# Optimization experiments

Hardware: AMD Instinct MI355X
Metric: run time of the kernel (lower is better)

Reference implementation:

```python
import jax, jax.numpy as jnp
import numpy as np

B, H, W, C = 4, 64, 64, 96
EXPAND = 2
D_INNER = EXPAND * C  # 192
N = 16   # d_state
K = 4    # scan directions
DT_RANK = int(np.ceil(C / 16))  # 6


def setup_inputs() -> dict:
    key = jax.random.key(0)
    ks = jax.random.split(key, 8)
    def rn(k, shape, scale=0.02):
        return jax.random.normal(k, shape, dtype=jnp.float32) * scale
    return {
        "x": jax.random.normal(ks[0], (B, H, W, C), dtype=jnp.float32),
        "ln_g": jnp.ones((C,), jnp.float32),
        "ln_b": jnp.zeros((C,), jnp.float32),
        "in_proj_w": rn(ks[1], (C, 2 * D_INNER)),
        "in_proj_b": jnp.zeros((2 * D_INNER,), jnp.float32),
        "conv_w": rn(ks[2], (D_INNER, 1, 3, 3), 0.1),
        "conv_b": jnp.zeros((D_INNER,), jnp.float32),
        "x_proj_w": rn(ks[3], (K, DT_RANK + 2 * N, D_INNER)),
        "dt_proj_w": rn(ks[4], (K, D_INNER, DT_RANK), 0.1),
        "dt_proj_b": rn(ks[5], (K, D_INNER), 0.1),
        "A_logs": jnp.log(jnp.tile(jnp.arange(1, N + 1, dtype=jnp.float32)[None, :], (K * D_INNER, 1))),
        "Ds": jnp.ones((K * D_INNER,), jnp.float32),
        "out_norm_g": jnp.ones((D_INNER,), jnp.float32),
        "out_norm_b": jnp.zeros((D_INNER,), jnp.float32),
        "out_proj_w": rn(ks[6], (D_INNER, C)),
        "out_proj_b": jnp.zeros((C,), jnp.float32),
    }


def _ln(x, g, b, eps):
    mu = x.mean(-1, keepdims=True)
    var = jnp.mean((x - mu) ** 2, axis=-1, keepdims=True)
    return (x - mu) * jax.lax.rsqrt(var + eps) * g + b


def _vss_forward(x, ln_g, ln_b, in_proj_w, in_proj_b, conv_w, conv_b,
                 x_proj_w, dt_proj_w, dt_proj_b, A_logs, Ds,
                 out_norm_g, out_norm_b, out_proj_w, out_proj_b):
    Bb, Hh, Ww, Cc = x.shape
    L = Hh * Ww
    d = D_INNER
    # ln_1 (eps=1e-6), then SS2D on channels-first layout
    xn = _ln(x, ln_g, ln_b, 1e-6)
    xz = jnp.einsum('bhwc,ce->bhwe', xn, in_proj_w) + in_proj_b
    xi, z = jnp.split(xz, 2, axis=-1)
    xi = xi.transpose(0, 3, 1, 2)  # (B, d, H, W)
    xi = jax.lax.conv_general_dilated(
        xi, conv_w, (1, 1), 'SAME', feature_group_count=d,
        dimension_numbers=('NCHW', 'OIHW', 'NCHW'))
    xi = jax.nn.silu(xi + conv_b[None, :, None, None])
    # 4 scan directions: row-major, col-major, and their reverses
    x_hw = xi.reshape(Bb, d, L)
    x_wh = xi.transpose(0, 1, 3, 2).reshape(Bb, d, L)
    xs = jnp.stack([x_hw, x_wh], axis=1)                      # (B,2,d,L)
    xs = jnp.concatenate([xs, jnp.flip(xs, axis=-1)], axis=1)  # (B,K,d,L)
    x_dbl = jnp.einsum('bkdl,kcd->bkcl', xs, x_proj_w)         # (B,K,R+2N,L)
    dt_r = x_dbl[:, :, :DT_RANK]
    Bs = x_dbl[:, :, DT_RANK:DT_RANK + N]                      # (B,K,N,L)
    Cs = x_dbl[:, :, DT_RANK + N:]                             # (B,K,N,L)
    dts = jnp.einsum('bkrl,kdr->bkdl', dt_r, dt_proj_w)
    dts = jax.nn.softplus(dts + dt_proj_b[None, :, :, None])
    A = -jnp.exp(A_logs).reshape(K, d, N)
    Dsk = Ds.reshape(K, d)

    def step(h, inp):
        u_t, dt_t, B_t, C_t = inp                  # (B,K,d),(B,K,d),(B,K,N),(B,K,N)
        dA = jnp.exp(dt_t[..., None] * A)          # (B,K,d,N)
        h = dA * h + (dt_t * u_t)[..., None] * B_t[:, :, None, :]
        y = jnp.einsum('bkdn,bkn->bkd', h, C_t)
        return h, y

    seq = (xs.transpose(3, 0, 1, 2), dts.transpose(3, 0, 1, 2),
           Bs.transpose(3, 0, 1, 2), Cs.transpose(3, 0, 1, 2))
    h0 = jnp.zeros((Bb, K, d, N), xs.dtype)
    _, ys = jax.lax.scan(step, h0, seq)            # ys: (L,B,K,d)
    ys = ys.transpose(1, 2, 3, 0)                  # (B,K,d,L)
    ys = ys + Dsk[None, :, :, None] * xs
    # merge the 4 directions back into one row-major map
    inv_y = jnp.flip(ys[:, 2:4], axis=-1)
    wh_y = ys[:, 1].reshape(Bb, d, Ww, Hh).transpose(0, 1, 3, 2).reshape(Bb, d, L)
    invwh_y = inv_y[:, 1].reshape(Bb, d, Ww, Hh).transpose(0, 1, 3, 2).reshape(Bb, d, L)
    y = ys[:, 0] + inv_y[:, 0] + wh_y + invwh_y    # (B,d,L)
    y = y.transpose(0, 2, 1).reshape(Bb, Hh, Ww, d)
    y = _ln(y, out_norm_g, out_norm_b, 1e-5)
    y = y * jax.nn.silu(z)
    out = jnp.einsum('bhwd,dc->bhwc', y, out_proj_w) + out_proj_b
    return x + out  # residual (drop_path = 0 -> identity)


def reference(x, ln_g, ln_b, in_proj_w, in_proj_b, conv_w, conv_b, x_proj_w,
              dt_proj_w, dt_proj_b, A_logs, Ds, out_norm_g, out_norm_b,
              out_proj_w, out_proj_b):
    return _vss_forward(x, ln_g, ln_b, in_proj_w, in_proj_b, conv_w, conv_b,
                        x_proj_w, dt_proj_w, dt_proj_b, A_logs, Ds,
                        out_norm_g, out_norm_b, out_proj_w, out_proj_b)
```

## Files before the change

### kernel.cpp

```cpp
#include <hip/hip_runtime.h>
#include <math.h>

#define CC   96
#define DIN  192
#define NST  16
#define KDIR 4
#define DTR  6
#define LL   4096
#define BB   4
#define NSEG 128
#define SEGLEN 32
#define XROW 40

#define SZ_BLD ((long)BB*LL*DIN)

__device__ __forceinline__ float sigmoidf_(float x){
    return __builtin_amdgcn_rcpf(1.0f + __expf(-x));
}
__device__ __forceinline__ int whmap(int l){ return ((l & 63) << 6) | (l >> 6); }

__device__ __forceinline__ void dt_and_E(float s, float& dt, float& E){
    const float LOG2E = 1.4426950408889634f;
    const float LN2   = 0.6931471805599453f;
    float sn  = s * LOG2E;
    float t   = __builtin_amdgcn_exp2f(-fabsf(sn));
    float opt = 1.0f + t;
    float r   = __builtin_amdgcn_rcpf(opt);
    E  = (s > 0.f) ? t*r : r;
    dt = LN2 * (fmaxf(sn, 0.f) + __builtin_amdgcn_logf(opt));
}
__device__ __forceinline__ void pow_tree(float E, float* En){
    En[0]=E;
    float E2=E*E;        En[1]=E2;
    En[2]=E2*E;  float E4=E2*E2; En[3]=E4;
    En[4]=E4*E;  En[5]=E4*E2;  En[6]=E4*En[2];
    float E8=E4*E4;      En[7]=E8;
    En[8]=E8*E;  En[9]=E8*E2;  En[10]=E8*En[2]; En[11]=E8*E4;
    En[12]=E8*En[4]; En[13]=E8*En[5]; En[14]=E8*En[6]; En[15]=E8*E8;
}
__device__ __forceinline__ void dir_base(int k, int lg0, int& p0, int& stride){
    switch(k & 3){
        case 0:  p0 = lg0;               stride = 1;   break;
        case 1:  p0 = whmap(lg0);        stride = 64;  break;
        case 2:  p0 = LL - 1 - lg0;      stride = -1;  break;
        default: p0 = whmap(LL-1-lg0);   stride = -64; break;
    }
}

__global__ __launch_bounds__(192) void kA(const float* __restrict__ x,
        const float* __restrict__ lng, const float* __restrict__ lnb,
        const float* __restrict__ W,   const float* __restrict__ bias,
        float* __restrict__ xi, float* __restrict__ z)
{
    __shared__ float xn[16*96];
    __shared__ float sc1[192], sc2[192];
    __shared__ float mu[16], rs[16];
    int t = threadIdx.x;
    long row0 = (long)blockIdx.x * 16;

    for(int q=t; q<16*96; q+=192) xn[q] = x[row0*96 + q];
    __syncthreads();
    {
        int r = t/12, i = t%12;
        float4 v0 = *(const float4*)(&xn[r*96 + i*8]);
        float4 v1 = *(const float4*)(&xn[r*96 + i*8 + 4]);
        float s  = v0.x+v0.y+v0.z+v0.w + v1.x+v1.y+v1.z+v1.w;
        float ss = v0.x*v0.x+v0.y*v0.y+v0.z*v0.z+v0.w*v0.w
                 + v1.x*v1.x+v1.y*v1.y+v1.z*v1.z+v1.w*v1.w;
        sc1[t]=s; sc2[t]=ss;
        __syncthreads();
        if(t<16){
            float S=0.f, SS=0.f;
            for(int j=0;j<12;j++){ S+=sc1[t*12+j]; SS+=sc2[t*12+j]; }
            float m = S*(1.0f/96.0f);
            float var = SS*(1.0f/96.0f) - m*m;
            mu[t]=m; rs[t]=rsqrtf(var + 1e-6f);
        }
        __syncthreads();
    }
    for(int q=t; q<16*96; q+=192){
        int r=q/96, c=q%96;
        xn[q] = (xn[q]-mu[r])*rs[r]*lng[c] + lnb[c];
    }
    __syncthreads();

    float acc0[16], acc1[16];
    #pragma unroll
    for(int r=0;r<16;r++){ acc0[r]=0.f; acc1[r]=0.f; }
    for(int c0=0; c0<96; c0+=4){
        float4 xv[16];
        #pragma unroll
        for(int r=0;r<16;r++) xv[r] = *(const float4*)(&xn[r*96 + c0]);
        #pragma unroll
        for(int j=0;j<4;j++){
            float w0 = W[(c0+j)*384 + t];
            float w1 = W[(c0+j)*384 + t + 192];
            #pragma unroll
            for(int r=0;r<16;r++){
                float xvj = (j==0)?xv[r].x:(j==1)?xv[r].y:(j==2)?xv[r].z:xv[r].w;
                acc0[r] = fmaf(xvj, w0, acc0[r]);
                acc1[r] = fmaf(xvj, w1, acc1[r]);
            }
        }
    }
    float b0 = bias[t], b1 = bias[t+192];
    #pragma unroll
    for(int r=0;r<16;r++){
        xi[(row0+r)*DIN + t] = acc0[r] + b0;
        z [(row0+r)*DIN + t] = acc1[r] + b1;
    }
}

__global__ __launch_bounds__(256) void kB(const float* __restrict__ xi,
        const float* __restrict__ cw, const float* __restrict__ cb,
        float* __restrict__ xc)
{
    long idx = (long)blockIdx.x*256 + threadIdx.x;
    if(idx >= SZ_BLD) return;
    int d = (int)(idx % DIN);
    long rg = idx / DIN;
    int p = (int)(rg % LL); int b = (int)(rg / LL);
    int h = p >> 6, w = p & 63;
    float acc = 0.f;
    #pragma unroll
    for(int dh=0; dh<3; dh++){
        int hh = h + dh - 1;
        if(hh < 0 || hh >= 64) continue;
        #pragma unroll
        for(int dw=0; dw<3; dw++){
            int ww2 = w + dw - 1;
            if(ww2 < 0 || ww2 >= 64) continue;
            acc = fmaf(xi[((long)b*LL + hh*64 + ww2)*DIN + d], cw[d*9 + dh*3 + dw], acc);
        }
    }
    acc += cb[d];
    xc[idx] = acc * sigmoidf_(acc);
}

__global__ __launch_bounds__(320) void kC(const float* __restrict__ xc,
        const float* __restrict__ xw, float* __restrict__ xdbl)
{
    __shared__ float ls[16*192];
    int t = threadIdx.x;
    long row0 = (long)blockIdx.x * 16;
    int b  = (int)(row0 / LL);
    int p0 = (int)(row0 % LL);
    for(int q=t; q<16*192; q+=320) ls[q] = xc[row0*DIN + q];
    __syncthreads();
    if(t < 304){
        int q4 = t / 76;
        int j  = t % 76;
        int k  = j / 38;
        int c  = j % 38;
        const float* wr0 = xw + (long)( k      *38 + c)*192;
        const float* wr1 = xw + (long)((k + 2) *38 + c)*192;
        float acc0[4], acc1[4];
        #pragma unroll
        for(int r=0;r<4;r++){ acc0[r]=0.f; acc1[r]=0.f; }
        int rbase = q4*4;
        for(int d=0; d<192; d+=4){
            float4 w0 = *(const float4*)(wr0 + d);
            float4 w1 = *(const float4*)(wr1 + d);
            #pragma unroll
            for(int r=0;r<4;r++){
                float4 lv = *(const float4*)(&ls[(rbase+r)*192 + d]);
                acc0[r] = fmaf(lv.x,w0.x, fmaf(lv.y,w0.y, fmaf(lv.z,w0.z, fmaf(lv.w,w0.w, acc0[r]))));
                acc1[r] = fmaf(lv.x,w1.x, fmaf(lv.y,w1.y, fmaf(lv.z,w1.z, fmaf(lv.w,w1.w, acc1[r]))));
            }
        }
        int cs = (c < 6) ? c : c + 2;
        long base0 = (long)(b*KDIR + k)*LL;
        long base2 = (long)(b*KDIR + k + 2)*LL;
        #pragma unroll
        for(int r=0;r<4;r++){
            int p  = p0 + rbase + r;
            int lk = (k==0) ? p : whmap(p);
            xdbl[(base0 + lk)*XROW + cs]            = acc0[r];
            xdbl[(base2 + (LL-1-lk))*XROW + cs]     = acc1[r];
        }
    }
}

__global__ __launch_bounds__(192) void kD2(const float* __restrict__ xc,
        const float* __restrict__ xdbl, const float* __restrict__ alog,
        const float* __restrict__ dtw,  const float* __restrict__ dtb,
        float* __restrict__ hend, float* __restrict__ dtsum)
{
    __shared__ float rows[SEGLEN*XROW];
    int t = threadIdx.x;
    int blk = blockIdx.x;
    int bk = blk / NSEG, seg = blk % NSEG;
    int b = bk / KDIR, k = bk % KDIR;
    {
        const float* src = xdbl + ((long)bk*LL + seg*SEGLEN)*XROW;
        for(int q=t; q<SEGLEN*XROW; q+=192) rows[q] = src[q];
    }
    int d = t, kd = k*192 + d;
    float a[16]; bool fast = true;
    #pragma unroll
    for(int n=0;n<16;n++){
        a[n] = -__expf(alog[kd*16 + n]);
        fast = fast && (fabsf(a[n] + (float)(n+1)) < 1e-3f);
    }
    float w6[6];
    #pragma unroll
    for(int r=0;r<6;r++) w6[r] = dtw[kd*6 + r];
    float bdt = dtb[kd];

    int lg0 = seg * SEGLEN;
    int p0, stride; dir_base(k, lg0, p0, stride);
    long addr  = ((long)b*LL + p0)*DIN + d;
    long astep = (long)stride*DIN;

    float h[16];
    #pragma unroll
    for(int n=0;n<16;n++) h[n]=0.f;
    float sdt = 0.f;
    __syncthreads();

    float u = xc[addr];
    for(int i=0; i<SEGLEN; i++){
        const float* row = &rows[i*XROW];
        float s = bdt;
        #pragma unroll
        for(int r=0;r<6;r++) s = fmaf(row[r], w6[r], s);
        float dt, E; dt_and_E(s, dt, E);
        sdt += dt;
        float wi = dt * u;
        float unext = 0.f;
        long addrN = addr + astep;
        if(i+1 < SEGLEN) unext = xc[addrN];
        float En[16];
        if(fast){ pow_tree(E, En); }
        else {
            #pragma unroll
            for(int n=0;n<16;n++) En[n] = __expf(dt * a[n]);
        }
        float Bv[16];
        #pragma unroll
        for(int n=0;n<16;n+=4) *(float4*)(Bv+n) = *(const float4*)(row + 8 + n);
        #pragma unroll
        for(int n=0;n<16;n++) h[n] = fmaf(En[n], h[n], wi*Bv[n]);
        addr = addrN; u = unext;
    }
    long hb = (((long)bk*NSEG + seg)*192 + d)*16;
    #pragma unroll
    for(int n=0;n<16;n+=4)
        *(float4*)(&hend[hb+n]) = make_float4(h[n],h[n+1],h[n+2],h[n+3]);
    dtsum[((long)bk*NSEG + seg)*192 + d] = sdt;
}

__global__ __launch_bounds__(256) void kE3(const float* __restrict__ alog,
        const float* __restrict__ dtsum, float* __restrict__ hx)
{
    int tid = blockIdx.x*256 + threadIdx.x;
    int c     = tid & 15;
    int chain = tid >> 4;
    int n  = chain & 15;
    int d  = (chain >> 4) % 192;
    int bk = chain / 3072;
    int k  = bk & 3;
    float an = -__expf(alog[(k*192 + d)*16 + n]);
    long sbase = (long)bk*NSEG*192  + d;
    long hbase = (long)bk*NSEG*3072 + d*16 + n;
    int seg0 = c*8;

    float P[8], he[8];
    #pragma unroll
    for(int i=0;i<8;i++){
        float sd = dtsum[sbase + (long)(seg0+i)*192];
        he[i]    = hx[hbase + (long)(seg0+i)*3072];
        P[i]     = __expf(an * sd);
    }
    float Pc = 1.f, Hc = 0.f;
    #pragma unroll
    for(int i=0;i<8;i++){
        Hc = fmaf(P[i], Hc, he[i]);
        Pc *= P[i];
    }
    #pragma unroll
    for(int dist=1; dist<16; dist<<=1){
        float Pp = __shfl_up(Pc, dist, 16);
        float Hp = __shfl_up(Hc, dist, 16);
        if(c >= dist){
            Hc = fmaf(Pc, Hp, Hc);
            Pc *= Pp;
        }
    }
    float H = __shfl_up(Hc, 1, 16);
    if(c == 0) H = 0.f;
    #pragma unroll
    for(int i=0;i<8;i++){
        hx[hbase + (long)(seg0+i)*3072] = H;
        H = fmaf(P[i], H, he[i]);
    }
}

__global__ __launch_bounds__(192) void kF2(const float* __restrict__ xc,
        const float* __restrict__ xdbl, const float* __restrict__ alog,
        const float* __restrict__ dtw,  const float* __restrict__ dtb,
        const float* __restrict__ Ds,   const float* __restrict__ Hprev,
        float* __restrict__ ys0, float* __restrict__ ys123)
{
    __shared__ float rows[SEGLEN*XROW];
    int t = threadIdx.x;
    int blk = blockIdx.x;
    int bk = blk / NSEG, seg = blk % NSEG;
    int b = bk / KDIR, k = bk % KDIR;
    {
        const float* src = xdbl + ((long)bk*LL + seg*SEGLEN)*XROW;
        for(int q=t; q<SEGLEN*XROW; q+=192) rows[q] = src[q];
    }
    int d = t, kd = k*192 + d;
    float a[16]; bool fast = true;
    #pragma unroll
    for(int n=0;n<16;n++){
        a[n] = -__expf(alog[kd*16 + n]);
        fast = fast && (fabsf(a[n] + (float)(n+1)) < 1e-3f);
    }
    float w6[6];
    #pragma unroll
    for(int r=0;r<6;r++) w6[r] = dtw[kd*6 + r];
    float bdt = dtb[kd];
    float Dd  = Ds[kd];
    float h[16];
    long hb = (((long)bk*NSEG + seg)*192 + d)*16;
    #pragma unroll
    for(int n=0;n<16;n+=4){
        float4 v = *(const float4*)(&Hprev[hb+n]);
        h[n]=v.x; h[n+1]=v.y; h[n+2]=v.z; h[n+3]=v.w;
    }
    float* ybuf = (k==0) ? ys0 : (ys123 + (long)(k-1)*SZ_BLD);

    int lg0 = seg * SEGLEN;
    int p0, stride; dir_base(k, lg0, p0, stride);
    long addr  = ((long)b*LL + p0)*DIN + d;
    long astep = (long)stride*DIN;
    __syncthreads();

    float u = xc[addr];
    for(int i=0; i<SEGLEN; i++){
        const float* row = &rows[i*XROW];
        float s = bdt;
        #pragma unroll
        for(int r=0;r<6;r++) s = fmaf(row[r], w6[r], s);
        float dt, E; dt_and_E(s, dt, E);
        float wi = dt * u;
        float unext = 0.f;
        long addrN = addr + astep;
        if(i+1 < SEGLEN) unext = xc[addrN];
        float En[16];
        if(fast){ pow_tree(E, En); }
        else {
            #pragma unroll
            for(int n=0;n<16;n++) En[n] = __expf(dt * a[n]);
        }
        float Bv[16], Cv[16];
        #pragma unroll
        for(int n=0;n<16;n+=4){
            *(float4*)(Bv+n) = *(const float4*)(row + 8 + n);
            *(float4*)(Cv+n) = *(const float4*)(row + 24 + n);
        }
        float y = Dd * u;
        #pragma unroll
        for(int n=0;n<16;n++){
            h[n] = fmaf(En[n], h[n], wi*Bv[n]);
            y = fmaf(h[n], Cv[n], y);
        }
        ybuf[addr] = y;
        addr = addrN; u = unext;
    }
}

__global__ __launch_bounds__(384) void kG(const float* __restrict__ ys0,
        const float* __restrict__ ys123, const float* __restrict__ z,
        const float* __restrict__ ong, const float* __restrict__ onb,
        const float* __restrict__ Wout, const float* __restrict__ ob,
        const float* __restrict__ x, float* __restrict__ out)
{
    __shared__ float yb[16*192];
    __shared__ float sc1[384], sc2[384];
    __shared__ float mu[16], rs[16];
    int t = threadIdx.x;
    long row0 = (long)blockIdx.x * 16;

    for(int q=t; q<3072; q+=384){
        long off = row0*DIN + q;
        yb[q] = ys0[off] + ys123[off] + ys123[SZ_BLD + off] + ys123[2*SZ_BLD + off];
    }
    __syncthreads();
    {
        int r = t/24, i = t%24;
        float s=0.f, ss=0.f;
        #pragma unroll
        for(int j=0;j<8;j++){ float v = yb[r*192 + i*8 + j]; s+=v; ss+=v*v; }
        sc1[t]=s; sc2[t]=ss;
        __syncthreads();
        if(t<16){
            float S=0.f, SS=0.f;
            for(int j=0;j<24;j++){ S+=sc1[t*24+j]; SS+=sc2[t*24+j]; }
            float m = S*(1.0f/192.0f);
            float var = SS*(1.0f/192.0f) - m*m;
            mu[t]=m; rs[t]=rsqrtf(var + 1e-5f);
        }
        __syncthreads();
    }
    for(int q=t; q<3072; q+=384){
        int r=q/192, dd=q%192;
        float v = (yb[q]-mu[r])*rs[r]*ong[dd] + onb[dd];
        float zz = z[row0*DIN + q];
        yb[q] = v * (zz * sigmoidf_(zz));
    }
    __syncthreads();
    int c = t % 96, rg4 = t / 96;
    float acc[4] = {0.f,0.f,0.f,0.f};
    for(int dd=0; dd<192; dd++){
        float wv = Wout[dd*96 + c];
        #pragma unroll
        for(int j=0;j<4;j++) acc[j] = fmaf(yb[(rg4*4+j)*192 + dd], wv, acc[j]);
    }
    float bv = ob[c];
    for(int j=0;j<4;j++){
        long row = row0 + rg4*4 + j;
        out[row*96 + c] = x[row*96 + c] + acc[j] + bv;
    }
}

extern "C" void kernel_launch(void* const* d_in, const int* in_sizes, int n_in,
                              void* d_out, int out_size, void* d_ws, size_t ws_size,
                              hipStream_t stream)
{
    const float* x    = (const float*)d_in[0];
    const float* lng  = (const float*)d_in[1];
    const float* lnb  = (const float*)d_in[2];
    const float* ipw  = (const float*)d_in[3];
    const float* ipb  = (const float*)d_in[4];
    const float* cw   = (const float*)d_in[5];
    const float* cb   = (const float*)d_in[6];
    const float* xpw  = (const float*)d_in[7];
    const float* dtw  = (const float*)d_in[8];
    const float* dtb  = (const float*)d_in[9];
    const float* alog = (const float*)d_in[10];
    const float* Ds   = (const float*)d_in[11];
    const float* ong  = (const float*)d_in[12];
    const float* onb  = (const float*)d_in[13];
    const float* opw  = (const float*)d_in[14];
    const float* opb  = (const float*)d_in[15];

    float* ws    = (float*)d_ws;
    float* xi    = ws + 0;
    float* z     = ws + 3145728;
    float* xc    = ws + 6291456;
    float* xdbl  = ws + 9437184;
    float* ys123 = ws + 12058624;
    float* hx    = ws + 21495808;
    float* dtsum = ws + 27787264;
    float* ys0   = xi;
    float* out   = (float*)d_out;

    hipLaunchKernelGGL(kA,  dim3(1024),  dim3(192), 0, stream, x, lng, lnb, ipw, ipb, xi, z);
    hipLaunchKernelGGL(kB,  dim3(12288), dim3(256), 0, stream, xi, cw, cb, xc);
    hipLaunchKernelGGL(kC,  dim3(1024),  dim3(320), 0, stream, xc, xpw, xdbl);
    hipLaunchKernelGGL(kD2, dim3(2048),  dim3(192), 0, stream, xc, xdbl, alog, dtw, dtb,
                       hx, dtsum);
    hipLaunchKernelGGL(kE3, dim3(3072),  dim3(256), 0, stream, alog, dtsum, hx);
    hipLaunchKernelGGL(kF2, dim3(2048),  dim3(192), 0, stream, xc, xdbl, alog, dtw, dtb,
                       Ds, hx, ys0, ys123);
    hipLaunchKernelGGL(kG,  dim3(1024),  dim3(384), 0, stream, ys0, ys123, z, ong, onb,
                       opw, opb, x, out);
}
```

Measured before the change: 328.4 us.

## Transpose x_proj weights and retile kC for coalesced weight loads

Adds a small kernel that transposes the x_proj weight into a [k][d][c] layout, so adjacent threads in kC read adjacent weight elements. kC is retiled to 8 rows per block with 152 active threads, each computing one (direction, channel) output over 8 rows instead of two directions over 4 rows. The aim is coalesced weight reads and higher occupancy, at the cost of an extra launch each call and of dropping the float4 weight loads.

After: 312.1 us. 1.05x faster.

```diff
diff --git a/kernel.cpp b/kernel.cpp
--- a/kernel.cpp
+++ b/kernel.cpp
@@ -45,6 +45,17 @@
         case 2:  p0 = LL - 1 - lg0;      stride = -1;  break;
         default: p0 = whmap(LL-1-lg0);   stride = -64; break;
     }
+}
+
+__global__ __launch_bounds__(256) void kT(const float* __restrict__ xw,
+                                          float* __restrict__ xwt)
+{
+    int tid = blockIdx.x*256 + threadIdx.x;
+    if(tid >= KDIR*38*192) return;
+    int d  = tid % 192;
+    int kc = tid / 192;
+    int k  = kc / 38, c = kc % 38;
+    xwt[((long)k*192 + d)*38 + c] = xw[tid];
 }
 
 __global__ __launch_bounds__(192) void kA(const float* __restrict__ x,
@@ -137,46 +148,43 @@
     xc[idx] = acc * sigmoidf_(acc);
 }
 
-__global__ __launch_bounds__(320) void kC(const float* __restrict__ xc,
-        const float* __restrict__ xw, float* __restrict__ xdbl)
-{
-    __shared__ float ls[16*192];
+__global__ __launch_bounds__(192) void kC(const float* __restrict__ xc,
+        const float* __restrict__ xwt, float* __restrict__ xdbl)
+{
+    __shared__ float ls[8*192];
     int t = threadIdx.x;
-    long row0 = (long)blockIdx.x * 16;
+    long row0 = (long)blockIdx.x * 8;
     int b  = (int)(row0 / LL);
     int p0 = (int)(row0 % LL);
-    for(int q=t; q<16*192; q+=320) ls[q] = xc[row0*DIN + q];
-    __syncthreads();
-    if(t < 304){
-        int q4 = t / 76;
-        int j  = t % 76;
-        int k  = j / 38;
-        int c  = j % 38;
-        const float* wr0 = xw + (long)( k      *38 + c)*192;
-        const float* wr1 = xw + (long)((k + 2) *38 + c)*192;
-        float acc0[4], acc1[4];
-        #pragma unroll
-        for(int r=0;r<4;r++){ acc0[r]=0.f; acc1[r]=0.f; }
-        int rbase = q4*4;
+    for(int q=t; q<8*192; q+=192) ls[q] = xc[row0*DIN + q];
+    __syncthreads();
+    if(t < 152){
+        int k = t/38, c = t%38;
+        const float* wt = xwt + (long)k*192*38 + c;
+        float acc[8];
+        #pragma unroll
+        for(int r=0;r<8;r++) acc[r]=0.f;
         for(int d=0; d<192; d+=4){
-            float4 w0 = *(const float4*)(wr0 + d);
-            float4 w1 = *(const float4*)(wr1 + d);
+            float w0 = wt[(d+0)*38];
+            float w1 = wt[(d+1)*38];
+            float w2 = wt[(d+2)*38];
+            float w3 = wt[(d+3)*38];
             #pragma unroll
-            for(int r=0;r<4;r++){
-                float4 lv = *(const float4*)(&ls[(rbase+r)*192 + d]);
-                acc0[r] = fmaf(lv.x,w0.x, fmaf(lv.y,w0.y, fmaf(lv.z,w0.z, fmaf(lv.w,w0.w, acc0[r]))));
-                acc1[r] = fmaf(lv.x,w1.x, fmaf(lv.y,w1.y, fmaf(lv.z,w1.z, fmaf(lv.w,w1.w, acc1[r]))));
+            for(int r=0;r<8;r++){
+                float4 lv = *(const float4*)(&ls[r*192 + d]);
+                acc[r] = fmaf(lv.x,w0, fmaf(lv.y,w1, fmaf(lv.z,w2, fmaf(lv.w,w3, acc[r]))));
             }
         }
         int cs = (c < 6) ? c : c + 2;
-        long base0 = (long)(b*KDIR + k)*LL;
-        long base2 = (long)(b*KDIR + k + 2)*LL;
-        #pragma unroll
-        for(int r=0;r<4;r++){
-            int p  = p0 + rbase + r;
-            int lk = (k==0) ? p : whmap(p);
-            xdbl[(base0 + lk)*XROW + cs]            = acc0[r];
-            xdbl[(base2 + (LL-1-lk))*XROW + cs]     = acc1[r];
+        #pragma unroll
+        for(int r=0;r<8;r++){
+            int p = p0 + r;
+            int lk;
+            if(k==0) lk = p;
+            else if(k==1) lk = whmap(p);
+            else if(k==2) lk = LL-1-p;
+            else lk = LL-1-whmap(p);
+            xdbl[(((long)(b*KDIR + k)*LL + lk)*XROW) + cs] = acc[r];
         }
     }
 }
@@ -455,12 +463,14 @@
     float* ys123 = ws + 12058624;
     float* hx    = ws + 21495808;
     float* dtsum = ws + 27787264;
+    float* xwt   = ws + 28180480;
     float* ys0   = xi;
     float* out   = (float*)d_out;
 
+    hipLaunchKernelGGL(kT,  dim3(114),   dim3(256), 0, stream, xpw, xwt);
     hipLaunchKernelGGL(kA,  dim3(1024),  dim3(192), 0, stream, x, lng, lnb, ipw, ipb, xi, z);
     hipLaunchKernelGGL(kB,  dim3(12288), dim3(256), 0, stream, xi, cw, cb, xc);
-    hipLaunchKernelGGL(kC,  dim3(1024),  dim3(320), 0, stream, xc, xpw, xdbl);
+    hipLaunchKernelGGL(kC,  dim3(2048),  dim3(192), 0, stream, xc, xwt, xdbl);
     hipLaunchKernelGGL(kD2, dim3(2048),  dim3(192), 0, stream, xc, xdbl, alog, dtw, dtb,
                        hx, dtsum);
     hipLaunchKernelGGL(kE3, dim3(3072),  dim3(256), 0, stream, alog, dtsum, hx);
```
